# Kernel tuning notes

Measured on AMD Instinct MI355X. Metric: run time of the kernel, lower is better.

## Reference

```python
import jax, jax.numpy as jnp
import numpy as np
from jax import lax

GAMMA = 0.99
LAM = 0.95
LN_EPS = 1e-5  # torch.nn.LayerNorm default

T = 524288      # buffer_size (timesteps)
D = 64          # state_space_shape
H = 256         # hidden_layer_sizes
A = 18          # action_space_size


def _layernorm(x, g, b):
    mu = jnp.mean(x, axis=-1, keepdims=True)
    var = jnp.mean((x - mu) ** 2, axis=-1, keepdims=True)
    return (x - mu) * lax.rsqrt(var + LN_EPS) * g + b


def _body(x, w1, b1, g1, n1, w2, b2, g2, n2, w3, b3):
    # Linear -> LayerNorm -> ReLU, twice, then final Linear
    h = jax.nn.relu(_layernorm(x @ w1 + b1, g1, n1))
    h = jax.nn.relu(_layernorm(h @ w2 + b2, g2, n2))
    return h @ w3 + b3


def _gae(deltas, masks):
    # advantages[i] = deltas[i] + gamma*lam*masks[i] * advantages[i+1], scanned in reverse
    coefs = (GAMMA * LAM) * masks

    def step(g, dc):
        d, c = dc
        g = d + c * g
        return g, g

    _, adv_rev = lax.scan(step, jnp.zeros((), deltas.dtype), (deltas[::-1], coefs[::-1]))
    return adv_rev[::-1]


def setup_inputs() -> dict:
    key = jax.random.key(0)
    ks = jax.random.split(key, 20)

    def w(k, shape, fan_in):
        return jax.random.normal(k, shape, jnp.float32) * (1.0 / np.sqrt(fan_in))

    inp = {
        "states": jax.random.normal(ks[0], (T, D), jnp.float32),
        "next_states": jax.random.normal(ks[1], (T, D), jnp.float32),
        "rewards": jax.random.normal(ks[2], (T,), jnp.float32),
        # masks = 1 - dones: mostly 1, occasional 0 at episode boundaries
        "masks": (jax.random.uniform(ks[3], (T,)) > 0.002).astype(jnp.float32),
        # actor params
        "aw1": w(ks[4], (D, H), D), "ab1": jnp.zeros((H,), jnp.float32),
        "ag1": jnp.ones((H,), jnp.float32), "an1": jnp.zeros((H,), jnp.float32),
        "aw2": w(ks[5], (H, H), H), "ab2": jnp.zeros((H,), jnp.float32),
        "ag2": jnp.ones((H,), jnp.float32), "an2": jnp.zeros((H,), jnp.float32),
        "aw3": w(ks[6], (H, A), H), "ab3": jnp.zeros((A,), jnp.float32),
        # critic params
        "cw1": w(ks[7], (D, H), D), "cb1": jnp.zeros((H,), jnp.float32),
        "cg1": jnp.ones((H,), jnp.float32), "cn1": jnp.zeros((H,), jnp.float32),
        "cw2": w(ks[8], (H, H), H), "cb2": jnp.zeros((H,), jnp.float32),
        "cg2": jnp.ones((H,), jnp.float32), "cn2": jnp.zeros((H,), jnp.float32),
        "cw3": w(ks[9], (H, 1), H), "cb3": jnp.zeros((1,), jnp.float32),
    }
    return inp


def reference(states, next_states, rewards, masks,
              aw1, ab1, ag1, an1, aw2, ab2, ag2, an2, aw3, ab3,
              cw1, cb1, cg1, cn1, cw2, cb2, cg2, cn2, cw3, cb3):
    # actor: probs over actions (Softmax(dim=-1))
    logits = _body(states, aw1, ab1, ag1, an1, aw2, ab2, ag2, an2, aw3, ab3)
    probs = jax.nn.softmax(logits, axis=-1)                     # [T, A]
    # critic values for states and next_states (.squeeze())
    values = _body(states, cw1, cb1, cg1, cn1, cw2, cb2, cg2, cn2, cw3, cb3)[:, 0]
    next_values = _body(next_states, cw1, cb1, cg1, cn1, cw2, cb2, cg2, cn2, cw3, cb3)[:, 0]
    # GAE
    deltas = rewards + GAMMA * next_values * masks - values     # [T]
    advantages = _gae(deltas, masks)                            # [T]
    returns = advantages + values                               # [T]
    # single packed output [T, A+2]
    return jnp.concatenate([probs, advantages[:, None], returns[:, None]], axis=-1)
```

## Files before the change

### kernel.cpp

```cpp
#include <hip/hip_runtime.h>
#include <hip/hip_bf16.h>


#define T_SZ 524288
#define GL 0.9405f

typedef __attribute__((ext_vector_type(8))) short bf16x8;
typedef __attribute__((ext_vector_type(4))) float f32x4;

#define OFF_AW1T 0
#define OFF_AW2T 16384
#define OFF_AW3T 81920
#define OFF_CW1T 90112
#define OFF_CW2T 106496
#define OFF_CW3T 172032
#define W_ELEMS  176128
#define OFF_DELTAS_BYTES 352256

__device__ __forceinline__ int perm_k(int k) {
  return (k & ~31) | ((k & 15) << 1) | ((k >> 4) & 1);
}

__device__ __forceinline__ unsigned pack2(float a, float b) {
  __hip_bfloat162 h = __float22bfloat162_rn(float2{a, b});
  union { __hip_bfloat162 h2; unsigned u; } x;
  x.h2 = h;
  return x.u;
}

__device__ __forceinline__ void unpack2(unsigned u, float& a, float& b) {
  union { unsigned u; float f; } x, y;
  x.u = u << 16; y.u = u & 0xFFFF0000u;
  a = x.f; b = y.f;
}

__device__ __forceinline__ void stage_x(const float* __restrict__ src,
                                        char* XB, int c, int q) {
  const float* rp = src + (size_t)c * 64;
#pragma unroll
  for (int ks = 0; ks < 2; ++ks) {
    float4 a = *(const float4*)(rp + ks * 32 + 4 * q);
    float4 b = *(const float4*)(rp + ks * 32 + 4 * q + 16);
    unsigned u[4];
    u[0] = pack2(a.x, b.x); u[1] = pack2(a.y, b.y);
    u[2] = pack2(a.z, b.z); u[3] = pack2(a.w, b.w);
    *(uint4*)(XB + c * 128 + ((ks * 64 + q * 16) ^ ((c & 7) << 4))) = *(uint4*)u;
  }
}

template<int K, int UNR>
__device__ __forceinline__ void layer1t(const char* A, int astr,
    const char* __restrict__ W, const float* PF, char* O,
    int c, int q, int lane) {
  constexpr int NK = K / 32;
  float s[4] = {0, 0, 0, 0}, ss[4] = {0, 0, 0, 0};
  const int sw = (c & 7) << 4;
#pragma unroll UNR
  for (int g = 0; g < 8; ++g) {
    const char* We = W + (size_t)(2 * g) * (K * 32);
    const char* Wo = We + (size_t)(K * 32);
    f32x4 e = {0.f, 0.f, 0.f, 0.f}, o = {0.f, 0.f, 0.f, 0.f};
#pragma unroll
    for (int ks = 0; ks < NK; ++ks) {
      bf16x8 be = *(const bf16x8*)(We + ks * 1024 + lane * 16);
      bf16x8 bo = *(const bf16x8*)(Wo + ks * 1024 + lane * 16);
      bf16x8 a = *(const bf16x8*)(A + (size_t)c * astr + ((ks * 64 + q * 16) ^ sw));
      e = __builtin_amdgcn_mfma_f32_16x16x32_bf16(a, be, e, 0, 0, 0);
      o = __builtin_amdgcn_mfma_f32_16x16x32_bf16(a, bo, o, 0, 0, 0);
    }
    const float bbe = PF[2 * g * 16 + c];
    const float bbo = PF[(2 * g + 1) * 16 + c];
#pragma unroll
    for (int r = 0; r < 4; ++r) {
      float ve = e[r] + bbe, vo = o[r] + bbo;
      s[r] += ve + vo; ss[r] += ve * ve + vo * vo;
      const int rsw = ((q * 4 + r) & 7) << 4;
      *(unsigned*)(O + (q * 4 + r) * 512 + ((g * 64 + c * 4) ^ rsw)) = pack2(ve, vo);
    }
  }
#pragma unroll
  for (int m = 1; m < 16; m <<= 1) {
#pragma unroll
    for (int r = 0; r < 4; ++r) {
      s[r] += __shfl_xor(s[r], m, 64);
      ss[r] += __shfl_xor(ss[r], m, 64);
    }
  }
#pragma unroll
  for (int r = 0; r < 4; ++r) {
    float mu = s[r] * (1.f / 256.f);
    ss[r] = rsqrtf(ss[r] * (1.f / 256.f) - mu * mu + 1e-5f); s[r] = mu;
  }
#pragma unroll
  for (int p = 0; p < 8; ++p) {
    const float g0 = PF[256 + p * 32 + c],      b0v = PF[512 + p * 32 + c];
    const float g1 = PF[256 + p * 32 + 16 + c], b1v = PF[512 + p * 32 + 16 + c];
#pragma unroll
    for (int r = 0; r < 4; ++r) {
      unsigned* ap = (unsigned*)(O + (q * 4 + r) * 512 +
                                 ((p * 64 + c * 4) ^ (((q * 4 + r) & 7) << 4)));
      float v0, v1;
      unpack2(*ap, v0, v1);
      v0 = fmaxf((v0 - s[r]) * ss[r] * g0 + b0v, 0.f);
      v1 = fmaxf((v1 - s[r]) * ss[r] * g1 + b1v, 0.f);
      *ap = pack2(v0, v1);
    }
  }
}

template<int NT>
__device__ __forceinline__ void run_small1(const char* A,
    const char* __restrict__ W, int c, int q, int lane, f32x4* o) {
  const int sw = (c & 7) << 4;
#pragma unroll
  for (int nt = 0; nt < NT; ++nt) o[nt] = (f32x4){0.f, 0.f, 0.f, 0.f};
#pragma unroll
  for (int nt = 0; nt < NT; ++nt) {
    const char* Wn = W + (size_t)nt * 8192;
#pragma unroll
    for (int ks = 0; ks < 8; ++ks) {
      bf16x8 b = *(const bf16x8*)(Wn + ks * 1024 + lane * 16);
      bf16x8 a = *(const bf16x8*)(A + (size_t)c * 512 + ((ks * 64 + q * 16) ^ sw));
      o[nt] = __builtin_amdgcn_mfma_f32_16x16x32_bf16(a, b, o[nt], 0, 0, 0);
    }
  }
}

__device__ __forceinline__ void softmax_write(f32x4* acc3,
    const float* __restrict__ ab3, float* __restrict__ out,
    int grow0, int c, int q) {
  float b0 = ab3[c];
  float b1 = (c < 2) ? ab3[16 + c] : 0.f;
#pragma unroll
  for (int r = 0; r < 4; ++r) {
    float x0 = acc3[0][r] + b0;
    float x1 = (c < 2) ? (acc3[1][r] + b1) : -1e30f;
    float mx = fmaxf(x0, x1);
#pragma unroll
    for (int m = 1; m < 16; m <<= 1) mx = fmaxf(mx, __shfl_xor(mx, m, 64));
    float e0 = __expf(x0 - mx);
    float e1 = (c < 2) ? __expf(x1 - mx) : 0.f;
    float sm = e0 + e1;
#pragma unroll
    for (int m = 1; m < 16; m <<= 1) sm += __shfl_xor(sm, m, 64);
    float inv = 1.f / sm;
    int gr = grow0 + q * 4 + r;
    out[(size_t)gr * 20 + c] = e0 * inv;
    if (c < 2) out[(size_t)gr * 20 + 16 + c] = e1 * inv;
  }
}

__device__ __forceinline__ int frag_idx(int mo, int K, int n, int k) {
  const int kp = perm_k(k);
  const int nt = n >> 4, cc = n & 15;
  const int ks = kp >> 5, w = kp & 31, qq = w >> 3, e = w & 7;
  return mo + nt * (16 * K) + ks * 512 + (qq * 16 + cc) * 8 + e;
}

__global__ void prep_weights(const float* __restrict__ aw1, const float* __restrict__ aw2,
                             const float* __restrict__ aw3, const float* __restrict__ cw1,
                             const float* __restrict__ cw2, const float* __restrict__ cw3,
                             __hip_bfloat16* __restrict__ wb) {
  int i = blockIdx.x * 256 + threadIdx.x;
  if (i >= W_ELEMS) return;
  float v; int dst;
  if (i < OFF_AW2T)      { int j = i;            int n = j >> 6, k = j & 63;  v = aw1[k * 256 + n];                 dst = frag_idx(OFF_AW1T, 64,  n, k); }
  else if (i < OFF_AW3T) { int j = i - OFF_AW2T; int n = j >> 8, k = j & 255; v = aw2[k * 256 + n];                 dst = frag_idx(OFF_AW2T, 256, n, k); }
  else if (i < OFF_CW1T) { int j = i - OFF_AW3T; int n = j >> 8, k = j & 255; v = (n < 18) ? aw3[k * 18 + n] : 0.f; dst = frag_idx(OFF_AW3T, 256, n, k); }
  else if (i < OFF_CW2T) { int j = i - OFF_CW1T; int n = j >> 6, k = j & 63;  v = cw1[k * 256 + n];                 dst = frag_idx(OFF_CW1T, 64,  n, k); }
  else if (i < OFF_CW3T) { int j = i - OFF_CW2T; int n = j >> 8, k = j & 255; v = cw2[k * 256 + n];                 dst = frag_idx(OFF_CW2T, 256, n, k); }
  else                   { int j = i - OFF_CW3T; int n = j >> 8, k = j & 255; v = (n == 0) ? cw3[k] : 0.f;          dst = frag_idx(OFF_CW3T, 256, n, k); }
  wb[dst] = __float2bfloat16(v);
}

__global__ __launch_bounds__(256, 2) void mlp_kernel(
    const float* __restrict__ states, const float* __restrict__ next_states,
    const float* __restrict__ rewards, const float* __restrict__ masks,
    const float* __restrict__ ab1, const float* __restrict__ ag1, const float* __restrict__ an1,
    const float* __restrict__ ab2, const float* __restrict__ ag2, const float* __restrict__ an2,
    const float* __restrict__ ab3,
    const float* __restrict__ cb1, const float* __restrict__ cg1, const float* __restrict__ cn1,
    const float* __restrict__ cb2, const float* __restrict__ cg2, const float* __restrict__ cn2,
    const float* __restrict__ cb3,
    const __hip_bfloat16* __restrict__ wbuf,
    float* __restrict__ deltas, float* __restrict__ out) {
  __shared__ char PB[12288];
  __shared__ char WV[4][16384];
  const int tid = threadIdx.x;
  const int wave = tid >> 6, lane = tid & 63;
  const int c = lane & 15, q = lane >> 4;
  char* A0 = WV[wave];
  char* A1 = WV[wave] + 8192;
  const char* W = (const char*)wbuf;
  const int base = blockIdx.x * 64 + wave * 16;

  {
    const float* bsrc = (wave == 0) ? ab1 : (wave == 1) ? ab2 : (wave == 2) ? cb1 : cb2;
    const float* gsrc = (wave == 0) ? ag1 : (wave == 1) ? ag2 : (wave == 2) ? cg1 : cg2;
    const float* nsrc = (wave == 0) ? an1 : (wave == 1) ? an2 : (wave == 2) ? cn1 : cn2;
    char* dst = PB + wave * 3072;
    *(float4*)(dst + lane * 16)        = *(const float4*)(bsrc + lane * 4);
    *(float4*)(dst + 1024 + lane * 16) = *(const float4*)(gsrc + lane * 4);
    *(float4*)(dst + 2048 + lane * 16) = *(const float4*)(nsrc + lane * 4);
  }
  __syncthreads();
  const float* PA1 = (const float*)(PB);
  const float* PA2 = (const float*)(PB + 3072);
  const float* PC1 = (const float*)(PB + 6144);
  const float* PC2 = (const float*)(PB + 9216);

  stage_x(states + (size_t)base * 64, A1, c, q);
  layer1t<64, 2>(A1, 128, W + OFF_AW1T * 2, PA1, A0, c, q, lane);
  __syncthreads();
  layer1t<256, 1>(A0, 512, W + OFF_AW2T * 2, PA2, A1, c, q, lane);
  __syncthreads();
  {
    f32x4 p3[2];
    run_small1<2>(A1, W + OFF_AW3T * 2, c, q, lane, p3);
    softmax_write(p3, ab3, out, base, c, q);
  }
  __syncthreads();

  stage_x(states + (size_t)base * 64, A1, c, q);
  layer1t<64, 2>(A1, 128, W + OFF_CW1T * 2, PC1, A0, c, q, lane);
  __syncthreads();
  layer1t<256, 1>(A0, 512, W + OFF_CW2T * 2, PC2, A1, c, q, lane);
  __syncthreads();
  float vst[4];
  {
    f32x4 v[1];
    run_small1<1>(A1, W + OFF_CW3T * 2, c, q, lane, v);
    const float b3 = cb3[0];
#pragma unroll
    for (int r = 0; r < 4; ++r) vst[r] = v[0][r] + b3;
  }
  __syncthreads();

  stage_x(next_states + (size_t)base * 64, A1, c, q);
  layer1t<64, 2>(A1, 128, W + OFF_CW1T * 2, PC1, A0, c, q, lane);
  __syncthreads();
  layer1t<256, 1>(A0, 512, W + OFF_CW2T * 2, PC2, A1, c, q, lane);
  __syncthreads();
  {
    f32x4 v[1];
    run_small1<1>(A1, W + OFF_CW3T * 2, c, q, lane, v);
    const float b3 = cb3[0];
    if (c == 0) {
#pragma unroll
      for (int r = 0; r < 4; ++r) {
        const int gr = base + q * 4 + r;
        const float nv = v[0][r] + b3;
        out[(size_t)gr * 20 + 19] = vst[r];
        deltas[gr] = rewards[gr] + 0.99f * nv * masks[gr] - vst[r];
      }
    }
  }
}

__global__ __launch_bounds__(256) void gae_kernel(
    const float* __restrict__ deltas, const float* __restrict__ masks,
    float* __restrict__ out) {
  const int w = (blockIdx.x * blockDim.x + threadIdx.x) >> 6;
  const int lane = threadIdx.x & 63;
  const int idx0 = w * 512 + lane * 16;

  float d[16], cf[16];
  if (idx0 < T_SZ) {
#pragma unroll
    for (int i = 0; i < 4; ++i) {
      *(float4*)(d + i * 4)  = *(const float4*)(deltas + idx0 + i * 4);
      *(float4*)(cf + i * 4) = *(const float4*)(masks + idx0 + i * 4);
    }
#pragma unroll
    for (int i = 0; i < 16; ++i) cf[i] *= GL;
  } else {
#pragma unroll
    for (int i = 0; i < 16; ++i) { d[i] = 0.f; cf[i] = 0.f; }
  }

  float A = 0.f, P = 1.f;
#pragma unroll
  for (int i = 15; i >= 0; --i) { A = d[i] + cf[i] * A; P *= cf[i]; }

  float As = A, Ps = P;
#pragma unroll
  for (int st = 1; st < 64; st <<= 1) {
    float An = __shfl_down(As, st, 64);
    float Pn = __shfl_down(Ps, st, 64);
    if (lane + st < 64) { As = As + Ps * An; Ps = Ps * Pn; }
  }
  float G = __shfl_down(As, 1, 64);
  if (lane == 63) G = 0.f;

  if (lane < 32) {
    float g = G;
#pragma unroll
    for (int i = 15; i >= 0; --i) {
      g = d[i] + cf[i] * g;
      const size_t j = (size_t)(idx0 + i);
      float val = out[j * 20 + 19];
      out[j * 20 + 18] = g;
      out[j * 20 + 19] = g + val;
    }
  }
}

extern "C" void kernel_launch(void* const* d_in, const int* in_sizes, int n_in,
                              void* d_out, int out_size, void* d_ws, size_t ws_size,
                              hipStream_t stream) {
  const float* states      = (const float*)d_in[0];
  const float* next_states = (const float*)d_in[1];
  const float* rewards     = (const float*)d_in[2];
  const float* masks       = (const float*)d_in[3];
  const float* aw1 = (const float*)d_in[4];
  const float* ab1 = (const float*)d_in[5];
  const float* ag1 = (const float*)d_in[6];
  const float* an1 = (const float*)d_in[7];
  const float* aw2 = (const float*)d_in[8];
  const float* ab2 = (const float*)d_in[9];
  const float* ag2 = (const float*)d_in[10];
  const float* an2 = (const float*)d_in[11];
  const float* aw3 = (const float*)d_in[12];
  const float* ab3 = (const float*)d_in[13];
  const float* cw1 = (const float*)d_in[14];
  const float* cb1 = (const float*)d_in[15];
  const float* cg1 = (const float*)d_in[16];
  const float* cn1 = (const float*)d_in[17];
  const float* cw2 = (const float*)d_in[18];
  const float* cb2 = (const float*)d_in[19];
  const float* cg2 = (const float*)d_in[20];
  const float* cn2 = (const float*)d_in[21];
  const float* cw3 = (const float*)d_in[22];
  const float* cb3 = (const float*)d_in[23];

  __hip_bfloat16* wbuf = (__hip_bfloat16*)d_ws;
  float* deltas = (float*)((char*)d_ws + OFF_DELTAS_BYTES);
  float* out = (float*)d_out;

  prep_weights<<<(W_ELEMS + 255) / 256, 256, 0, stream>>>(aw1, aw2, aw3, cw1, cw2, cw3, wbuf);
  mlp_kernel<<<T_SZ / 64, 256, 0, stream>>>(
      states, next_states, rewards, masks,
      ab1, ag1, an1, ab2, ag2, an2, ab3,
      cb1, cg1, cn1, cb2, cg2, cn2, cb3,
      wbuf, deltas, out);
  gae_kernel<<<256, 256, 0, stream>>>(deltas, masks, out);
}
```

Baseline: 788.2 us.

## Keep MLP activations in register MFMA fragments and halve per-wave LDS

Input states are packed directly into bf16 A-operand fragments in registers instead of staged through LDS, and each layer's LayerNorm+ReLU output is read back once into register fragments for the next layer's MFMAs. The critic reuses the already-loaded state fragments rather than reloading from global memory. The per-wave LDS scratch shrinks from two buffers to one, which could allow more blocks per CU. In exchange, register pressure rises because eight bf16x8 fragments stay live, and LayerNorm stats now need cross-lane shuffles to reach the transposed layout.

```diff
diff --git a/kernel.cpp b/kernel.cpp
--- a/kernel.cpp
+++ b/kernel.cpp
@@ -34,8 +34,12 @@
   a = x.f; b = y.f;
 }
 
-__device__ __forceinline__ void stage_x(const float* __restrict__ src,
-                                        char* XB, int c, int q) {
+__device__ __forceinline__ void* act_at(void* base, int row, int colByte) {
+  return (char*)base + row * 512 + (colByte ^ ((row & 7) << 4));
+}
+
+__device__ __forceinline__ void load_x_frags(const float* __restrict__ src,
+                                             int c, int q, bf16x8* xf) {
   const float* rp = src + (size_t)c * 64;
 #pragma unroll
   for (int ks = 0; ks < 2; ++ks) {
@@ -44,17 +48,16 @@
     unsigned u[4];
     u[0] = pack2(a.x, b.x); u[1] = pack2(a.y, b.y);
     u[2] = pack2(a.z, b.z); u[3] = pack2(a.w, b.w);
-    *(uint4*)(XB + c * 128 + ((ks * 64 + q * 16) ^ ((c & 7) << 4))) = *(uint4*)u;
+    xf[ks] = *(bf16x8*)u;
   }
 }
 
 template<int K, int UNR>
-__device__ __forceinline__ void layer1t(const char* A, int astr,
-    const char* __restrict__ W, const float* PF, char* O,
-    int c, int q, int lane) {
+__device__ __forceinline__ void layer_reg(const bf16x8* af,
+    const char* __restrict__ W, const float* PF, char* ACT,
+    int c, int q, int lane, bf16x8* of) {
   constexpr int NK = K / 32;
   float s[4] = {0, 0, 0, 0}, ss[4] = {0, 0, 0, 0};
-  const int sw = (c & 7) << 4;
 #pragma unroll UNR
   for (int g = 0; g < 8; ++g) {
     const char* We = W + (size_t)(2 * g) * (K * 32);
@@ -64,9 +67,8 @@
     for (int ks = 0; ks < NK; ++ks) {
       bf16x8 be = *(const bf16x8*)(We + ks * 1024 + lane * 16);
       bf16x8 bo = *(const bf16x8*)(Wo + ks * 1024 + lane * 16);
-      bf16x8 a = *(const bf16x8*)(A + (size_t)c * astr + ((ks * 64 + q * 16) ^ sw));
-      e = __builtin_amdgcn_mfma_f32_16x16x32_bf16(a, be, e, 0, 0, 0);
-      o = __builtin_amdgcn_mfma_f32_16x16x32_bf16(a, bo, o, 0, 0, 0);
+      e = __builtin_amdgcn_mfma_f32_16x16x32_bf16(af[ks], be, e, 0, 0, 0);
+      o = __builtin_amdgcn_mfma_f32_16x16x32_bf16(af[ks], bo, o, 0, 0, 0);
     }
     const float bbe = PF[2 * g * 16 + c];
     const float bbo = PF[(2 * g + 1) * 16 + c];
@@ -74,8 +76,7 @@
     for (int r = 0; r < 4; ++r) {
       float ve = e[r] + bbe, vo = o[r] + bbo;
       s[r] += ve + vo; ss[r] += ve * ve + vo * vo;
-      const int rsw = ((q * 4 + r) & 7) << 4;
-      *(unsigned*)(O + (q * 4 + r) * 512 + ((g * 64 + c * 4) ^ rsw)) = pack2(ve, vo);
+      *(unsigned*)act_at(ACT, q * 4 + r, g * 64 + c * 4) = pack2(ve, vo);
     }
   }
 #pragma unroll
@@ -86,32 +87,47 @@
       ss[r] += __shfl_xor(ss[r], m, 64);
     }
   }
+  float mean[4], rs[4];
 #pragma unroll
   for (int r = 0; r < 4; ++r) {
-    float mu = s[r] * (1.f / 256.f);
-    ss[r] = rsqrtf(ss[r] * (1.f / 256.f) - mu * mu + 1e-5f); s[r] = mu;
-  }
-#pragma unroll
-  for (int p = 0; p < 8; ++p) {
-    const float g0 = PF[256 + p * 32 + c],      b0v = PF[512 + p * 32 + c];
-    const float g1 = PF[256 + p * 32 + 16 + c], b1v = PF[512 + p * 32 + 16 + c];
-#pragma unroll
-    for (int r = 0; r < 4; ++r) {
-      unsigned* ap = (unsigned*)(O + (q * 4 + r) * 512 +
-                                 ((p * 64 + c * 4) ^ (((q * 4 + r) & 7) << 4)));
+    mean[r] = s[r] * (1.f / 256.f);
+    float var = ss[r] * (1.f / 256.f) - mean[r] * mean[r];
+    rs[r] = rsqrtf(var + 1e-5f);
+  }
+  const int srcLane = ((c >> 2) << 4) + c;
+  float mb[4], rb[4];
+#pragma unroll
+  for (int r = 0; r < 4; ++r) {
+    mb[r] = __shfl(mean[r], srcLane, 64);
+    rb[r] = __shfl(rs[r],   srcLane, 64);
+  }
+  const float m01 = (c & 1) ? mb[1] : mb[0], m23 = (c & 1) ? mb[3] : mb[2];
+  const float r01 = (c & 1) ? rb[1] : rb[0], r23 = (c & 1) ? rb[3] : rb[2];
+  const float mc = (c & 2) ? m23 : m01;
+  const float rc = (c & 2) ? r23 : r01;
+  const float* GM = PF + 256;
+  const float* BT = PF + 512;
+#pragma unroll
+  for (int ks = 0; ks < 8; ++ks) {
+    uint4 dv = *(const uint4*)act_at(ACT, c, ks * 64 + q * 16);
+    unsigned w[4];
+    const unsigned* dp = (const unsigned*)&dv;
+#pragma unroll
+    for (int i = 0; i < 4; ++i) {
+      const int n0 = ks * 32 + q * 4 + i;
       float v0, v1;
-      unpack2(*ap, v0, v1);
-      v0 = fmaxf((v0 - s[r]) * ss[r] * g0 + b0v, 0.f);
-      v1 = fmaxf((v1 - s[r]) * ss[r] * g1 + b1v, 0.f);
-      *ap = pack2(v0, v1);
-    }
+      unpack2(dp[i], v0, v1);
+      float w0 = fmaxf((v0 - mc) * rc * GM[n0]      + BT[n0],      0.f);
+      float w1 = fmaxf((v1 - mc) * rc * GM[n0 + 16] + BT[n0 + 16], 0.f);
+      w[i] = pack2(w0, w1);
+    }
+    of[ks] = *(bf16x8*)w;
   }
 }
 
 template<int NT>
-__device__ __forceinline__ void run_small1(const char* A,
-    const char* __restrict__ W, int c, int q, int lane, f32x4* o) {
-  const int sw = (c & 7) << 4;
+__device__ __forceinline__ void run_small_reg(const bf16x8* af,
+    const char* __restrict__ W, int lane, f32x4* o) {
 #pragma unroll
   for (int nt = 0; nt < NT; ++nt) o[nt] = (f32x4){0.f, 0.f, 0.f, 0.f};
 #pragma unroll
@@ -120,8 +136,7 @@
 #pragma unroll
     for (int ks = 0; ks < 8; ++ks) {
       bf16x8 b = *(const bf16x8*)(Wn + ks * 1024 + lane * 16);
-      bf16x8 a = *(const bf16x8*)(A + (size_t)c * 512 + ((ks * 64 + q * 16) ^ sw));
-      o[nt] = __builtin_amdgcn_mfma_f32_16x16x32_bf16(a, b, o[nt], 0, 0, 0);
+      o[nt] = __builtin_amdgcn_mfma_f32_16x16x32_bf16(af[ks], b, o[nt], 0, 0, 0);
     }
   }
 }
@@ -185,12 +200,11 @@
     const __hip_bfloat16* __restrict__ wbuf,
     float* __restrict__ deltas, float* __restrict__ out) {
   __shared__ char PB[12288];
-  __shared__ char WV[4][16384];
+  __shared__ char WV[4][8192];
   const int tid = threadIdx.x;
   const int wave = tid >> 6, lane = tid & 63;
   const int c = lane & 15, q = lane >> 4;
-  char* A0 = WV[wave];
-  char* A1 = WV[wave] + 8192;
+  char* ACT = WV[wave];
   const char* W = (const char*)wbuf;
   const int base = blockIdx.x * 64 + wave * 16;
 
@@ -209,41 +223,43 @@
   const float* PC1 = (const float*)(PB + 6144);
   const float* PC2 = (const float*)(PB + 9216);
 
-  stage_x(states + (size_t)base * 64, A1, c, q);
-  layer1t<64, 2>(A1, 128, W + OFF_AW1T * 2, PA1, A0, c, q, lane);
-  __syncthreads();
-  layer1t<256, 1>(A0, 512, W + OFF_AW2T * 2, PA2, A1, c, q, lane);
+  bf16x8 xf[2], af[8];
+
+  load_x_frags(states + (size_t)base * 64, c, q, xf);
+
+  layer_reg<64, 2>(xf, W + OFF_AW1T * 2, PA1, ACT, c, q, lane, af);
+  __syncthreads();
+  layer_reg<256, 1>(af, W + OFF_AW2T * 2, PA2, ACT, c, q, lane, af);
   __syncthreads();
   {
     f32x4 p3[2];
-    run_small1<2>(A1, W + OFF_AW3T * 2, c, q, lane, p3);
+    run_small_reg<2>(af, W + OFF_AW3T * 2, lane, p3);
     softmax_write(p3, ab3, out, base, c, q);
   }
   __syncthreads();
 
-  stage_x(states + (size_t)base * 64, A1, c, q);
-  layer1t<64, 2>(A1, 128, W + OFF_CW1T * 2, PC1, A0, c, q, lane);
-  __syncthreads();
-  layer1t<256, 1>(A0, 512, W + OFF_CW2T * 2, PC2, A1, c, q, lane);
+  layer_reg<64, 2>(xf, W + OFF_CW1T * 2, PC1, ACT, c, q, lane, af);
+  __syncthreads();
+  layer_reg<256, 1>(af, W + OFF_CW2T * 2, PC2, ACT, c, q, lane, af);
   __syncthreads();
   float vst[4];
   {
     f32x4 v[1];
-    run_small1<1>(A1, W + OFF_CW3T * 2, c, q, lane, v);
+    run_small_reg<1>(af, W + OFF_CW3T * 2, lane, v);
     const float b3 = cb3[0];
 #pragma unroll
     for (int r = 0; r < 4; ++r) vst[r] = v[0][r] + b3;
   }
   __syncthreads();
 
-  stage_x(next_states + (size_t)base * 64, A1, c, q);
-  layer1t<64, 2>(A1, 128, W + OFF_CW1T * 2, PC1, A0, c, q, lane);
-  __syncthreads();
-  layer1t<256, 1>(A0, 512, W + OFF_CW2T * 2, PC2, A1, c, q, lane);
+  load_x_frags(next_states + (size_t)base * 64, c, q, xf);
+  layer_reg<64, 2>(xf, W + OFF_CW1T * 2, PC1, ACT, c, q, lane, af);
+  __syncthreads();
+  layer_reg<256, 1>(af, W + OFF_CW2T * 2, PC2, ACT, c, q, lane, af);
   __syncthreads();
   {
     f32x4 v[1];
-    run_small1<1>(A1, W + OFF_CW3T * 2, c, q, lane, v);
+    run_small_reg<1>(af, W + OFF_CW3T * 2, lane, v);
     const float b3 = cb3[0];
     if (c == 0) {
 #pragma unroll
```

Result: faster. 653.9 us (-17.0%).
